# Kernel optimization log

Hardware: AMD Instinct MI355X
Metric: run time of the kernel (lower is better)

Reference implementation:

```python
import jax, jax.numpy as jnp
import numpy as np

N = 50000      # nodes
E = 800000     # edges
IN = 128       # in_feats
HID = 16       # h_feats (per head)
HEADS = 8      # num_heads layer 1
CLS = 40       # num_classes
NEG_SLOPE = 0.2


def setup_inputs() -> dict:
    key = jax.random.key(0)
    ks = jax.random.split(key, 12)
    s = lambda fan: np.float32(1.0 / np.sqrt(fan))
    return {
        "features": jax.random.normal(ks[0], (N, IN), jnp.float32),
        "edge_src": jax.random.randint(ks[1], (E,), 0, N, dtype=jnp.int32),
        "edge_dst": jax.random.randint(ks[2], (E,), 0, N, dtype=jnp.int32),
        # layer 1 params
        "W1": jax.random.normal(ks[3], (IN, HEADS * HID), jnp.float32) * s(IN),
        "al1": jax.random.normal(ks[4], (HEADS, HID), jnp.float32) * s(HID),
        "ar1": jax.random.normal(ks[5], (HEADS, HID), jnp.float32) * s(HID),
        "b1": jnp.zeros((HEADS * HID,), jnp.float32),
        # layer 2 params (1 head)
        "W2": jax.random.normal(ks[6], (HEADS * HID, CLS), jnp.float32) * s(HEADS * HID),
        "al2": jax.random.normal(ks[7], (1, CLS), jnp.float32) * s(CLS),
        "ar2": jax.random.normal(ks[8], (1, CLS), jnp.float32) * s(CLS),
        "b2": jnp.zeros((CLS,), jnp.float32),
    }


def gat_conv(x, W, al, ar, b, src, dst, heads, out_dim):
    # x: [N, F_in] -> feat: [N, H, D]
    feat = (x @ W).reshape(-1, heads, out_dim)
    el = (feat * al).sum(-1)                      # [N, H]
    er = (feat * ar).sum(-1)                      # [N, H]
    e = jax.nn.leaky_relu(el[src] + er[dst], NEG_SLOPE)  # [E, H]
    # segment softmax over destination neighborhoods
    emax = jax.ops.segment_max(e, dst, num_segments=N)   # [N, H]
    emax = jnp.where(jnp.isfinite(emax), emax, jnp.float32(0.0))
    ee = jnp.exp(e - emax[dst])                   # [E, H]
    denom = jax.ops.segment_sum(ee, dst, num_segments=N)
    alpha = ee / (denom[dst] + jnp.float32(1e-9)) # [E, H]
    msg = alpha[:, :, None] * feat[src]           # [E, H, D]
    out = jax.ops.segment_sum(msg, dst, num_segments=N)  # [N, H, D]
    return out + b.reshape(1, heads, out_dim)


def reference(features, edge_src, edge_dst, W1, al1, ar1, b1, W2, al2, ar2, b2):
    h = jax.nn.elu(gat_conv(features, W1, al1, ar1, b1, edge_src, edge_dst, HEADS, HID))
    h = h.reshape(N, HEADS * HID)                 # flatten(1)
    out = gat_conv(h, W2, al2, ar2, b2, edge_src, edge_dst, 1, CLS)
    return out.mean(axis=1)                       # [N, CLS]
```

## Files before the change

### kernel.cpp

```cpp
#include <hip/hip_runtime.h>
#include <hip/hip_bf16.h>

#define N_NODES 50000
#define N_EDGES 800000
#define IN_F    128
#define HID     16
#define HEADS   8
#define F1      128
#define CLS     40
#define CLSP    64
#define NEG     0.2f
#define NEG_INF (-__builtin_inff())
#define SLOT    64

#define GEMM1_BLOCKS ((N_NODES + 63) / 64)
#define SCAT_BLOCKS  ((N_EDGES + 255) / 256)

typedef __bf16 bf16x8 __attribute__((ext_vector_type(8)));
typedef float  f32x4  __attribute__((ext_vector_type(4)));
typedef float  f32x2  __attribute__((ext_vector_type(2)));

__device__ __forceinline__ float leaky(float v) { return v >= 0.0f ? v : NEG * v; }
__device__ __forceinline__ f32x2 unpk(unsigned u) {
    f32x2 r;
    r.x = __uint_as_float(u << 16);
    r.y = __uint_as_float(u & 0xffff0000u);
    return r;
}

__global__ void setup_kernel(const float* __restrict__ W1, const float* __restrict__ W2,
                             __bf16* __restrict__ w1t, __bf16* __restrict__ w2t,
                             int* __restrict__ cursor) {
    int i = blockIdx.x * blockDim.x + threadIdx.x;
    if (i < N_NODES) cursor[i] = 0;
    if (i < 128 * 128) {
        int n = i >> 7, k = i & 127;
        w1t[i] = (__bf16)W1[k * 128 + n];
    }
    if (i < CLSP * 128) {
        int n = i >> 7, k = i & 127;
        w2t[i] = (n < CLS) ? (__bf16)W2[k * CLS + n] : (__bf16)0.0f;
    }
}

__device__ __forceinline__ void gemm1_body(int bid, int tid,
                                           const float* __restrict__ A,
                                           const __bf16* __restrict__ Wt,
                                           const float* __restrict__ al1,
                                           const float* __restrict__ ar1,
                                           __bf16* __restrict__ outb,
                                           float* __restrict__ el,
                                           float* __restrict__ er) {
    int wave = tid >> 6, lane = tid & 63;
    int m0 = bid * 64 + wave * 16;
    int c = lane & 15;
    int row = m0 + c;
    int rowc = row < N_NODES ? row : N_NODES - 1;
    int ko = (lane >> 4) * 8;

    f32x4 acc[8];
    #pragma unroll
    for (int t = 0; t < 8; ++t)
        #pragma unroll
        for (int r = 0; r < 4; ++r) acc[t][r] = 0.f;

    for (int ks = 0; ks < 128; ks += 32) {
        const float* ap = A + (size_t)rowc * 128 + ks + ko;
        float4 u = *(const float4*)ap;
        float4 v = *(const float4*)(ap + 4);
        bf16x8 a;
        a[0] = (__bf16)u.x; a[1] = (__bf16)u.y; a[2] = (__bf16)u.z; a[3] = (__bf16)u.w;
        a[4] = (__bf16)v.x; a[5] = (__bf16)v.y; a[6] = (__bf16)v.z; a[7] = (__bf16)v.w;
        #pragma unroll
        for (int t = 0; t < 8; ++t) {
            bf16x8 b = *(const bf16x8*)(Wt + (size_t)(t * 16 + c) * 128 + ks + ko);
            acc[t] = __builtin_amdgcn_mfma_f32_16x16x32_bf16(a, b, acc[t], 0, 0, 0);
        }
    }
    int rbase = m0 + (lane >> 4) * 4;
    #pragma unroll
    for (int t = 0; t < 8; ++t) {
        int gcol = t * 16 + c;
        #pragma unroll
        for (int r = 0; r < 4; ++r) {
            int grow = rbase + r;
            if (grow < N_NODES) outb[(size_t)grow * 128 + gcol] = (__bf16)acc[t][r];
        }
    }
    #pragma unroll
    for (int t = 0; t < 8; ++t) {
        float alv = al1[t * 16 + c];
        float arv = ar1[t * 16 + c];
        float pe[4], pr[4];
        #pragma unroll
        for (int r = 0; r < 4; ++r) { pe[r] = acc[t][r] * alv; pr[r] = acc[t][r] * arv; }
        #pragma unroll
        for (int mask = 1; mask <= 8; mask <<= 1) {
            #pragma unroll
            for (int r = 0; r < 4; ++r) {
                pe[r] += __shfl_xor(pe[r], mask, 64);
                pr[r] += __shfl_xor(pr[r], mask, 64);
            }
        }
        if (c == 0) {
            #pragma unroll
            for (int r = 0; r < 4; ++r) {
                int grow = rbase + r;
                if (grow < N_NODES) {
                    el[grow * 8 + t] = pe[r];
                    er[grow * 8 + t] = pr[r];
                }
            }
        }
    }
}

__device__ __forceinline__ void scatter_body(int bid, int tid,
                                             const int* __restrict__ src,
                                             const int* __restrict__ dst,
                                             int* __restrict__ cursor,
                                             unsigned short* __restrict__ srcs16) {
    int e = bid * 256 + tid;
    if (e >= N_EDGES) return;
    int d = dst[e];
    int c = atomicAdd(&cursor[d], 1);
    if (c < SLOT) srcs16[d * SLOT + c] = (unsigned short)src[e];
}

__global__ __launch_bounds__(256) void fat_gemm1_scatter(const float* __restrict__ A,
                                                         const __bf16* __restrict__ Wt,
                                                         const float* __restrict__ al1,
                                                         const float* __restrict__ ar1,
                                                         __bf16* __restrict__ outb,
                                                         float* __restrict__ el,
                                                         float* __restrict__ er,
                                                         const int* __restrict__ esrc,
                                                         const int* __restrict__ edst,
                                                         int* __restrict__ cursor,
                                                         unsigned short* __restrict__ srcs16) {
    if (blockIdx.x < GEMM1_BLOCKS)
        gemm1_body(blockIdx.x, threadIdx.x, A, Wt, al1, ar1, outb, el, er);
    else
        scatter_body(blockIdx.x - GEMM1_BLOCKS, threadIdx.x, esrc, edst, cursor, srcs16);
}

__global__ __launch_bounds__(256) void gemm2_mfma(const __bf16* __restrict__ A,
                                                  const __bf16* __restrict__ Wt,
                                                  const float* __restrict__ al2,
                                                  const float* __restrict__ ar2,
                                                  __bf16* __restrict__ out,
                                                  float* __restrict__ el,
                                                  float* __restrict__ er) {
    int wave = threadIdx.x >> 6, lane = threadIdx.x & 63;
    int m0 = blockIdx.x * 64 + wave * 16;
    int c = lane & 15;
    int row = m0 + c;
    int rowc = row < N_NODES ? row : N_NODES - 1;
    int ko = (lane >> 4) * 8;

    f32x4 acc[4];
    #pragma unroll
    for (int t = 0; t < 4; ++t)
        #pragma unroll
        for (int r = 0; r < 4; ++r) acc[t][r] = 0.f;

    for (int ks = 0; ks < 128; ks += 32) {
        bf16x8 a = *(const bf16x8*)(A + (size_t)rowc * 128 + ks + ko);
        #pragma unroll
        for (int t = 0; t < 4; ++t) {
            bf16x8 b = *(const bf16x8*)(Wt + (size_t)(t * 16 + c) * 128 + ks + ko);
            acc[t] = __builtin_amdgcn_mfma_f32_16x16x32_bf16(a, b, acc[t], 0, 0, 0);
        }
    }
    int rbase = m0 + (lane >> 4) * 4;
    #pragma unroll
    for (int t = 0; t < 4; ++t) {
        int gcol = t * 16 + c;
        #pragma unroll
        for (int r = 0; r < 4; ++r) {
            int grow = rbase + r;
            if (grow < N_NODES) out[(size_t)grow * CLSP + gcol] = (__bf16)acc[t][r];
        }
    }
    float pe[4] = {0.f, 0.f, 0.f, 0.f}, pr[4] = {0.f, 0.f, 0.f, 0.f};
    #pragma unroll
    for (int t = 0; t < 3; ++t) {
        int idx = t * 16 + c;
        float alv = (idx < CLS) ? al2[idx] : 0.f;
        float arv = (idx < CLS) ? ar2[idx] : 0.f;
        #pragma unroll
        for (int r = 0; r < 4; ++r) { pe[r] += acc[t][r] * alv; pr[r] += acc[t][r] * arv; }
    }
    #pragma unroll
    for (int mask = 1; mask <= 8; mask <<= 1) {
        #pragma unroll
        for (int r = 0; r < 4; ++r) {
            pe[r] += __shfl_xor(pe[r], mask, 64);
            pr[r] += __shfl_xor(pr[r], mask, 64);
        }
    }
    if (c == 0) {
        #pragma unroll
        for (int r = 0; r < 4; ++r) {
            int grow = rbase + r;
            if (grow < N_NODES) { el[grow] = pe[r]; er[grow] = pr[r]; }
        }
    }
}

__global__ __launch_bounds__(256) void gat1_fused(const int* __restrict__ degs,
                                                  const unsigned short* __restrict__ srcs,
                                                  const float* __restrict__ el,
                                                  const float* __restrict__ er,
                                                  const __bf16* __restrict__ feat1b,
                                                  const float* __restrict__ b1,
                                                  __bf16* __restrict__ hbufb) {
    __shared__ float a_lds[4][64 * 8];
    __shared__ int   s_lds[4][64];
    int wave = threadIdx.x >> 6;
    int lane = threadIdx.x & 63;
    int d = blockIdx.x * 4 + wave;
    int off = d * SLOT;
    int deg = min(degs[d], SLOT);

    int h = lane & 7, slot = lane >> 3;
    int q = lane >> 4, fg = lane & 15, hd = fg >> 1;
    float er_d = er[d * 8 + h];

    f32x2 accv[4];
    #pragma unroll
    for (int j = 0; j < 4; ++j) { accv[j].x = 0.f; accv[j].y = 0.f; }

    int nit = (deg + 7) >> 3;
    float sc[8];
    int sreg[8];
    float m = NEG_INF;
    #pragma unroll
    for (int it = 0; it < 8; ++it) {
        float v = NEG_INF;
        int e = it * 8 + slot;
        if (it < nit && e < deg) {
            sreg[it] = (int)srcs[off + e];
            v = leaky(el[sreg[it] * 8 + h] + er_d);
        }
        sc[it] = v;
        m = fmaxf(m, v);
    }
    float l = 0.f;
    #pragma unroll
    for (int it = 0; it < 8; ++it)
        l += (sc[it] == NEG_INF) ? 0.f : __expf(sc[it] - m);
    #pragma unroll
    for (int mask = 8; mask <= 32; mask <<= 1) {
        float m2 = __shfl_xor(m, mask, 64);
        float l2 = __shfl_xor(l, mask, 64);
        float mn = fmaxf(m, m2);
        float f1 = (m  == NEG_INF) ? 0.f : __expf(m - mn);
        float f2 = (m2 == NEG_INF) ? 0.f : __expf(m2 - mn);
        l = l * f1 + l2 * f2;
        m = mn;
    }
    float inv_l = 1.f / (l + 1e-9f);
    #pragma unroll
    for (int it = 0; it < 8; ++it) {
        int e = it * 8 + slot;
        if (it < nit && e < deg) {
            a_lds[wave][e * 8 + h] = __expf(sc[it] - m) * inv_l;
            if (h == 0) s_lds[wave][e] = sreg[it];
        }
    }

    int ng = (deg + 3) >> 2;
    #pragma unroll 4
    for (int g = 0; g < ng; ++g) {
        int k = g * 4 + q;
        float a = 0.f;
        int se = 0;
        if (k < deg) {
            a = a_lds[wave][k * 8 + hd];
            se = s_lds[wave][k];
        }
        uint4 p = *(const uint4*)(feat1b + (size_t)se * F1 + fg * 8);
        f32x2 av; av.x = a; av.y = a;
        accv[0] += av * unpk(p.x);
        accv[1] += av * unpk(p.y);
        accv[2] += av * unpk(p.z);
        accv[3] += av * unpk(p.w);
    }

    float acc[8];
    #pragma unroll
    for (int j = 0; j < 4; ++j) { acc[2 * j] = accv[j].x; acc[2 * j + 1] = accv[j].y; }
    #pragma unroll
    for (int i = 0; i < 8; ++i) {
        acc[i] += __shfl_xor(acc[i], 16, 64);
        acc[i] += __shfl_xor(acc[i], 32, 64);
    }
    if (q == 0) {
        bf16x8 o;
        #pragma unroll
        for (int i = 0; i < 8; ++i) {
            float v = acc[i] + b1[fg * 8 + i];
            v = v > 0.f ? v : expm1f(v);
            o[i] = (__bf16)v;
        }
        *(bf16x8*)(hbufb + (size_t)d * F1 + fg * 8) = o;
    }
}

__global__ __launch_bounds__(256) void gat2_fused(const int* __restrict__ degs,
                                                  const unsigned short* __restrict__ srcs,
                                                  const float* __restrict__ el,
                                                  const float* __restrict__ er,
                                                  const __bf16* __restrict__ feat2p,
                                                  const float* __restrict__ b2,
                                                  float* __restrict__ out) {
    int wave = threadIdx.x >> 6;
    int lane = threadIdx.x & 63;
    int d = blockIdx.x * 4 + wave;
    int off = d * SLOT;
    int deg = min(degs[d], SLOT);

    float er_d = er[d];
    int q  = lane >> 4;
    int cg = lane & 15;
    f32x2 accv[2];
    accv[0].x = 0.f; accv[0].y = 0.f; accv[1].x = 0.f; accv[1].y = 0.f;

    float sc = NEG_INF;
    int s0 = 0;
    if (lane < deg) {
        s0 = (int)srcs[off + lane];
        sc = leaky(el[s0] + er_d);
    }
    float m = sc, l = (sc == NEG_INF) ? 0.f : 1.f;
    #pragma unroll
    for (int mask = 1; mask <= 32; mask <<= 1) {
        float m2 = __shfl_xor(m, mask, 64);
        float l2 = __shfl_xor(l, mask, 64);
        float mn = fmaxf(m, m2);
        float f1 = (m  == NEG_INF) ? 0.f : __expf(m - mn);
        float f2 = (m2 == NEG_INF) ? 0.f : __expf(m2 - mn);
        l = l * f1 + l2 * f2;
        m = mn;
    }
    float inv_l = 1.f / (l + 1e-9f);
    float alpha = (sc == NEG_INF) ? 0.f : __expf(sc - m) * inv_l;

    int nsub = (deg + 3) >> 2;
    #pragma unroll 4
    for (int sub = 0; sub < nsub; ++sub) {
        int k = sub * 4 + q;
        float a  = __shfl(alpha, k, 64);
        int   se = __shfl(s0,    k, 64);
        uint2 p = *(const uint2*)(feat2p + (size_t)se * CLSP + cg * 4);
        f32x2 av; av.x = a; av.y = a;
        accv[0] += av * unpk(p.x);
        accv[1] += av * unpk(p.y);
    }

    float acc[4];
    acc[0] = accv[0].x; acc[1] = accv[0].y; acc[2] = accv[1].x; acc[3] = accv[1].y;
    #pragma unroll
    for (int i = 0; i < 4; ++i) {
        acc[i] += __shfl_xor(acc[i], 16, 64);
        acc[i] += __shfl_xor(acc[i], 32, 64);
    }
    if (lane < 10) {
        float4 o;
        o.x = acc[0] + b2[cg * 4 + 0];
        o.y = acc[1] + b2[cg * 4 + 1];
        o.z = acc[2] + b2[cg * 4 + 2];
        o.w = acc[3] + b2[cg * 4 + 3];
        *(float4*)(out + (size_t)d * CLS + cg * 4) = o;
    }
}

extern "C" void kernel_launch(void* const* d_in, const int* in_sizes, int n_in,
                              void* d_out, int out_size, void* d_ws, size_t ws_size,
                              hipStream_t stream) {
    const float* features = (const float*)d_in[0];
    const int*   esrc     = (const int*)d_in[1];
    const int*   edst     = (const int*)d_in[2];
    const float* W1       = (const float*)d_in[3];
    const float* al1      = (const float*)d_in[4];
    const float* ar1      = (const float*)d_in[5];
    const float* b1       = (const float*)d_in[6];
    const float* W2       = (const float*)d_in[7];
    const float* al2      = (const float*)d_in[8];
    const float* ar2      = (const float*)d_in[9];
    const float* b2       = (const float*)d_in[10];
    float* out = (float*)d_out;

    float* ws = (float*)d_ws;
    float*          el1    = ws;
    float*          er1    = ws + 400000;
    float*          el2    = ws + 800000;
    float*          er2    = ws + 850000;
    int*            cursor = (int*)(ws + 900000);
    unsigned short* srcs16 = (unsigned short*)(ws + 950000);
    __bf16*         feat1b = (__bf16*)(ws + 2550000);
    __bf16*         hbufb  = (__bf16*)(ws + 5750000);
    __bf16*         feat2p = (__bf16*)(ws + 8950000);
    __bf16*         w1t    = (__bf16*)(ws + 10550000);
    __bf16*         w2t    = (__bf16*)(ws + 10558192);

    const int B = 256;

    setup_kernel<<<(N_NODES + B - 1) / B, B, 0, stream>>>(W1, W2, w1t, w2t, cursor);

    fat_gemm1_scatter<<<GEMM1_BLOCKS + SCAT_BLOCKS, B, 0, stream>>>(
        features, w1t, al1, ar1, feat1b, el1, er1, esrc, edst, cursor, srcs16);

    gat1_fused<<<N_NODES / 4, B, 0, stream>>>(cursor, srcs16, el1, er1, feat1b, b1, hbufb);

    gemm2_mfma<<<(N_NODES + 63) / 64, 256, 0, stream>>>(hbufb, w2t, al2, ar2,
                                                        feat2p, el2, er2);
    gat2_fused<<<N_NODES / 4, B, 0, stream>>>(cursor, srcs16, el2, er2, feat2p, b2, out);
}
```

Before: 261.9 us.

## Drop max-subtraction softmax pass and split fused gemm1/scatter kernel

The GAT aggregation kernels no longer compute a per-destination max and precomputed alpha via LDS or shuffles. They now accumulate exp(score)-weighted features and the denominator in a single pass, normalizing at the end. The fused gemm1+scatter launch is also split back into two separate kernels. This removes a full pre-pass over the edges, the LDS staging and the shuffle reductions, but exp without max subtraction can overflow when scores are large.

```diff
diff --git a/kernel.cpp b/kernel.cpp
--- a/kernel.cpp
+++ b/kernel.cpp
@@ -10,10 +10,8 @@
 #define CLS     40
 #define CLSP    64
 #define NEG     0.2f
-#define NEG_INF (-__builtin_inff())
 #define SLOT    64
 
-#define GEMM1_BLOCKS ((N_NODES + 63) / 64)
 #define SCAT_BLOCKS  ((N_EDGES + 255) / 256)
 
 typedef __bf16 bf16x8 __attribute__((ext_vector_type(8)));
@@ -43,16 +41,26 @@
     }
 }
 
-__device__ __forceinline__ void gemm1_body(int bid, int tid,
-                                           const float* __restrict__ A,
-                                           const __bf16* __restrict__ Wt,
-                                           const float* __restrict__ al1,
-                                           const float* __restrict__ ar1,
-                                           __bf16* __restrict__ outb,
-                                           float* __restrict__ el,
-                                           float* __restrict__ er) {
-    int wave = tid >> 6, lane = tid & 63;
-    int m0 = bid * 64 + wave * 16;
+__global__ __launch_bounds__(256) void scatter_kernel(const int* __restrict__ src,
+                                                      const int* __restrict__ dst,
+                                                      int* __restrict__ cursor,
+                                                      unsigned short* __restrict__ srcs16) {
+    int e = blockIdx.x * 256 + threadIdx.x;
+    if (e >= N_EDGES) return;
+    int d = dst[e];
+    int c = atomicAdd(&cursor[d], 1);
+    if (c < SLOT) srcs16[d * SLOT + c] = (unsigned short)src[e];
+}
+
+__global__ __launch_bounds__(256) void gemm1_mfma(const float* __restrict__ A,
+                                                  const __bf16* __restrict__ Wt,
+                                                  const float* __restrict__ al1,
+                                                  const float* __restrict__ ar1,
+                                                  __bf16* __restrict__ outb,
+                                                  float* __restrict__ el,
+                                                  float* __restrict__ er) {
+    int wave = threadIdx.x >> 6, lane = threadIdx.x & 63;
+    int m0 = blockIdx.x * 64 + wave * 16;
     int c = lane & 15;
     int row = m0 + c;
     int rowc = row < N_NODES ? row : N_NODES - 1;
@@ -113,35 +121,6 @@
             }
         }
     }
-}
-
-__device__ __forceinline__ void scatter_body(int bid, int tid,
-                                             const int* __restrict__ src,
-                                             const int* __restrict__ dst,
-                                             int* __restrict__ cursor,
-                                             unsigned short* __restrict__ srcs16) {
-    int e = bid * 256 + tid;
-    if (e >= N_EDGES) return;
-    int d = dst[e];
-    int c = atomicAdd(&cursor[d], 1);
-    if (c < SLOT) srcs16[d * SLOT + c] = (unsigned short)src[e];
-}
-
-__global__ __launch_bounds__(256) void fat_gemm1_scatter(const float* __restrict__ A,
-                                                         const __bf16* __restrict__ Wt,
-                                                         const float* __restrict__ al1,
-                                                         const float* __restrict__ ar1,
-                                                         __bf16* __restrict__ outb,
-                                                         float* __restrict__ el,
-                                                         float* __restrict__ er,
-                                                         const int* __restrict__ esrc,
-                                                         const int* __restrict__ edst,
-                                                         int* __restrict__ cursor,
-                                                         unsigned short* __restrict__ srcs16) {
-    if (blockIdx.x < GEMM1_BLOCKS)
-        gemm1_body(blockIdx.x, threadIdx.x, A, Wt, al1, ar1, outb, el, er);
-    else
-        scatter_body(blockIdx.x - GEMM1_BLOCKS, threadIdx.x, esrc, edst, cursor, srcs16);
 }
 
 __global__ __launch_bounds__(256) void gemm2_mfma(const __bf16* __restrict__ A,
@@ -215,73 +194,31 @@
                                                   const __bf16* __restrict__ feat1b,
                                                   const float* __restrict__ b1,
                                                   __bf16* __restrict__ hbufb) {
-    __shared__ float a_lds[4][64 * 8];
-    __shared__ int   s_lds[4][64];
     int wave = threadIdx.x >> 6;
     int lane = threadIdx.x & 63;
     int d = blockIdx.x * 4 + wave;
     int off = d * SLOT;
     int deg = min(degs[d], SLOT);
 
-    int h = lane & 7, slot = lane >> 3;
     int q = lane >> 4, fg = lane & 15, hd = fg >> 1;
-    float er_d = er[d * 8 + h];
+    float er_d = er[d * 8 + hd];
 
     f32x2 accv[4];
     #pragma unroll
     for (int j = 0; j < 4; ++j) { accv[j].x = 0.f; accv[j].y = 0.f; }
-
-    int nit = (deg + 7) >> 3;
-    float sc[8];
-    int sreg[8];
-    float m = NEG_INF;
-    #pragma unroll
-    for (int it = 0; it < 8; ++it) {
-        float v = NEG_INF;
-        int e = it * 8 + slot;
-        if (it < nit && e < deg) {
-            sreg[it] = (int)srcs[off + e];
-            v = leaky(el[sreg[it] * 8 + h] + er_d);
-        }
-        sc[it] = v;
-        m = fmaxf(m, v);
-    }
-    float l = 0.f;
-    #pragma unroll
-    for (int it = 0; it < 8; ++it)
-        l += (sc[it] == NEG_INF) ? 0.f : __expf(sc[it] - m);
-    #pragma unroll
-    for (int mask = 8; mask <= 32; mask <<= 1) {
-        float m2 = __shfl_xor(m, mask, 64);
-        float l2 = __shfl_xor(l, mask, 64);
-        float mn = fmaxf(m, m2);
-        float f1 = (m  == NEG_INF) ? 0.f : __expf(m - mn);
-        float f2 = (m2 == NEG_INF) ? 0.f : __expf(m2 - mn);
-        l = l * f1 + l2 * f2;
-        m = mn;
-    }
-    float inv_l = 1.f / (l + 1e-9f);
-    #pragma unroll
-    for (int it = 0; it < 8; ++it) {
-        int e = it * 8 + slot;
-        if (it < nit && e < deg) {
-            a_lds[wave][e * 8 + h] = __expf(sc[it] - m) * inv_l;
-            if (h == 0) s_lds[wave][e] = sreg[it];
-        }
-    }
+    float dsum = 0.f;
 
     int ng = (deg + 3) >> 2;
     #pragma unroll 4
     for (int g = 0; g < ng; ++g) {
         int k = g * 4 + q;
-        float a = 0.f;
-        int se = 0;
-        if (k < deg) {
-            a = a_lds[wave][k * 8 + hd];
-            se = s_lds[wave][k];
-        }
-        uint4 p = *(const uint4*)(feat1b + (size_t)se * F1 + fg * 8);
-        f32x2 av; av.x = a; av.y = a;
+        bool ok = k < deg;
+        int s = ok ? (int)srcs[off + k] : 0;
+        float elv = el[s * 8 + hd];
+        uint4 p = *(const uint4*)(feat1b + (size_t)s * F1 + fg * 8);
+        float w = ok ? __expf(leaky(elv + er_d)) : 0.f;
+        dsum += w;
+        f32x2 av; av.x = w; av.y = w;
         accv[0] += av * unpk(p.x);
         accv[1] += av * unpk(p.y);
         accv[2] += av * unpk(p.z);
@@ -296,11 +233,15 @@
         acc[i] += __shfl_xor(acc[i], 16, 64);
         acc[i] += __shfl_xor(acc[i], 32, 64);
     }
+    dsum += __shfl_xor(dsum, 16, 64);
+    dsum += __shfl_xor(dsum, 32, 64);
+    float inv_l = 1.f / (dsum + 1e-9f);
+
     if (q == 0) {
         bf16x8 o;
         #pragma unroll
         for (int i = 0; i < 8; ++i) {
-            float v = acc[i] + b1[fg * 8 + i];
+            float v = acc[i] * inv_l + b1[fg * 8 + i];
             v = v > 0.f ? v : expm1f(v);
             o[i] = (__bf16)v;
         }
@@ -326,35 +267,19 @@
     int cg = lane & 15;
     f32x2 accv[2];
     accv[0].x = 0.f; accv[0].y = 0.f; accv[1].x = 0.f; accv[1].y = 0.f;
-
-    float sc = NEG_INF;
-    int s0 = 0;
-    if (lane < deg) {
-        s0 = (int)srcs[off + lane];
-        sc = leaky(el[s0] + er_d);
-    }
-    float m = sc, l = (sc == NEG_INF) ? 0.f : 1.f;
-    #pragma unroll
-    for (int mask = 1; mask <= 32; mask <<= 1) {
-        float m2 = __shfl_xor(m, mask, 64);
-        float l2 = __shfl_xor(l, mask, 64);
-        float mn = fmaxf(m, m2);
-        float f1 = (m  == NEG_INF) ? 0.f : __expf(m - mn);
-        float f2 = (m2 == NEG_INF) ? 0.f : __expf(m2 - mn);
-        l = l * f1 + l2 * f2;
-        m = mn;
-    }
-    float inv_l = 1.f / (l + 1e-9f);
-    float alpha = (sc == NEG_INF) ? 0.f : __expf(sc - m) * inv_l;
-
-    int nsub = (deg + 3) >> 2;
+    float dsum = 0.f;
+
+    int ng = (deg + 3) >> 2;
     #pragma unroll 4
-    for (int sub = 0; sub < nsub; ++sub) {
-        int k = sub * 4 + q;
-        float a  = __shfl(alpha, k, 64);
-        int   se = __shfl(s0,    k, 64);
-        uint2 p = *(const uint2*)(feat2p + (size_t)se * CLSP + cg * 4);
-        f32x2 av; av.x = a; av.y = a;
+    for (int g = 0; g < ng; ++g) {
+        int k = g * 4 + q;
+        bool ok = k < deg;
+        int s = ok ? (int)srcs[off + k] : 0;
+        float elv = el[s];
+        uint2 p = *(const uint2*)(feat2p + (size_t)s * CLSP + cg * 4);
+        float w = ok ? __expf(leaky(elv + er_d)) : 0.f;
+        dsum += w;
+        f32x2 av; av.x = w; av.y = w;
         accv[0] += av * unpk(p.x);
         accv[1] += av * unpk(p.y);
     }
@@ -366,12 +291,16 @@
         acc[i] += __shfl_xor(acc[i], 16, 64);
         acc[i] += __shfl_xor(acc[i], 32, 64);
     }
+    dsum += __shfl_xor(dsum, 16, 64);
+    dsum += __shfl_xor(dsum, 32, 64);
+    float inv_l = 1.f / (dsum + 1e-9f);
+
     if (lane < 10) {
         float4 o;
-        o.x = acc[0] + b2[cg * 4 + 0];
-        o.y = acc[1] + b2[cg * 4 + 1];
-        o.z = acc[2] + b2[cg * 4 + 2];
-        o.w = acc[3] + b2[cg * 4 + 3];
+        o.x = acc[0] * inv_l + b2[cg * 4 + 0];
+        o.y = acc[1] * inv_l + b2[cg * 4 + 1];
+        o.z = acc[2] * inv_l + b2[cg * 4 + 2];
+        o.w = acc[3] * inv_l + b2[cg * 4 + 3];
         *(float4*)(out + (size_t)d * CLS + cg * 4) = o;
     }
 }
@@ -409,12 +338,15 @@
 
     setup_kernel<<<(N_NODES + B - 1) / B, B, 0, stream>>>(W1, W2, w1t, w2t, cursor);
 
-    fat_gemm1_scatter<<<GEMM1_BLOCKS + SCAT_BLOCKS, B, 0, stream>>>(
-        features, w1t, al1, ar1, feat1b, el1, er1, esrc, edst, cursor, srcs16);
+    scatter_kernel<<<SCAT_BLOCKS, B, 0, stream>>>(esrc, edst, cursor, srcs16);
+
+    gemm1_mfma<<<(N_NODES + 63) / 64, B, 0, stream>>>(features, w1t, al1, ar1,
+                                                      feat1b, el1, er1);
 
     gat1_fused<<<N_NODES / 4, B, 0, stream>>>(cursor, srcs16, el1, er1, feat1b, b1, hbufb);
 
-    gemm2_mfma<<<(N_NODES + 63) / 64, 256, 0, stream>>>(hbufb, w2t, al2, ar2,
-                                                        feat2p, el2, er2);
+    gemm2_mfma<<<(N_NODES + 63) / 64, B, 0, stream>>>(hbufb, w2t, al2, ar2,
+                                                      feat2p, el2, er2);
+
     gat2_fused<<<N_NODES / 4, B, 0, stream>>>(cursor, srcs16, el2, er2, feat2p, b2, out);
 }
```

After: 273.6 us. +4.5%, slower.
